# Optimization experiments

Hardware: AMD Instinct MI355X
Metric: run time of the kernel (lower is better)

The kernel has to match this reference:

```python
import jax, jax.numpy as jnp
import numpy as np

B, D_IN = 4096, 4096
TOTAL_NODES, OUT_NODES = 17384, 1000
HID = TOTAL_NODES - OUT_NODES  # 16384


def setup_inputs() -> dict:
    key = jax.random.key(0)
    k1, k2, k3, k4, k5 = jax.random.split(key, 5)
    s1 = 1.0 / np.sqrt(D_IN)
    s2 = 1.0 / np.sqrt(D_IN + HID)
    return {
        "x": jax.random.normal(k1, (B, D_IN), dtype=jnp.float32),
        "W1": jax.random.normal(k2, (HID, D_IN), dtype=jnp.float32) * s1,
        "b1": jax.random.normal(k3, (HID,), dtype=jnp.float32) * s1,
        "W2": jax.random.normal(k4, (OUT_NODES, D_IN + HID), dtype=jnp.float32) * s2,
        "b2": jax.random.normal(k5, (OUT_NODES,), dtype=jnp.float32) * s2,
    }


def reference(x, W1, b1, W2, b2):
    # layer1 + ReLU: [B, HID]
    h1 = jax.nn.relu(jnp.einsum("bd,hd->bh", x, W1) + b1)
    # concat input with hidden activations: [B, D_IN + HID]
    concat = jnp.concatenate([x, h1], axis=1)
    # layer2: [B, OUT_NODES]
    out = jnp.einsum("bc,oc->bo", concat, W2) + b2
    return out
```

## Files before the change

### kernel.cpp

```cpp
#include <hip/hip_runtime.h>
#include <cstdint>
#include <cstddef>


using u16 = unsigned short;

typedef __bf16 bf16x8 __attribute__((ext_vector_type(8)));
typedef float  f32x4  __attribute__((ext_vector_type(4)));

#define GLOBAL_AS __attribute__((address_space(1)))
#define LDS_AS    __attribute__((address_space(3)))

__device__ __forceinline__ void async_load16(const void* gp, void* lp) {
    __builtin_amdgcn_global_load_lds((GLOBAL_AS void*)gp, (LDS_AS void*)lp, 16, 0, 0);
}

__device__ __forceinline__ u16 f2bf(float f) {
    union { float f; uint32_t u; } c; c.f = f;
    uint32_t u = c.u;
    u += 0x7FFFu + ((u >> 16) & 1u);
    return (u16)(u >> 16);
}

__device__ __forceinline__ int swz(int q, int row) { return q ^ ((row >> 1) & 3); }


__global__ void cvt_x_kernel(const float* __restrict__ x, u16* __restrict__ dst) {
    int idx = blockIdx.x * 256 + threadIdx.x;
    int row = idx >> 10;
    int c4  = (idx & 1023) << 2;
    float4 v = *(const float4*)&x[(size_t)row * 4096 + c4];
    ushort4 o;
    o.x = f2bf(v.x); o.y = f2bf(v.y); o.z = f2bf(v.z); o.w = f2bf(v.w);
    *(ushort4*)&dst[(size_t)row * 20480 + c4] = o;
}

__global__ void cvt_flat_kernel(const float* __restrict__ src, u16* __restrict__ dst) {
    int idx = blockIdx.x * 256 + threadIdx.x;
    float4 v = *(const float4*)&src[(size_t)idx * 4];
    ushort4 o;
    o.x = f2bf(v.x); o.y = f2bf(v.y); o.z = f2bf(v.z); o.w = f2bf(v.w);
    *(ushort4*)&dst[(size_t)idx * 4] = o;
}

__global__ void cvt_w2_kernel(const float* __restrict__ src, u16* __restrict__ dst) {
    int idx = blockIdx.x * 256 + threadIdx.x;
    int row = idx / 5120;
    int c4  = (idx % 5120) * 4;
    ushort4 o;
    if (row < 1000) {
        float4 v = *(const float4*)&src[(size_t)row * 20480 + c4];
        o.x = f2bf(v.x); o.y = f2bf(v.y); o.z = f2bf(v.z); o.w = f2bf(v.w);
    } else {
        o.x = 0; o.y = 0; o.z = 0; o.w = 0;
    }
    *(ushort4*)&dst[(size_t)row * 20480 + c4] = o;
}

template <int EPI, int SWZ>
__global__ __launch_bounds__(512, 2)
void gemm256_kernel(const u16* __restrict__ A, int lda,
                    const u16* __restrict__ B, int ldb,
                    int K,
                    const float* __restrict__ bias,
                    void* __restrict__ Cout, int ldc, size_t c_slab) {
    __shared__ __align__(16) u16 As[4 * 8192];
    __shared__ __align__(16) u16 Bs[4 * 8192];

    const int tid = threadIdx.x;

    int bx = blockIdx.x, by = blockIdx.y;
    if (SWZ) {
        const int lin   = by * (int)gridDim.x + bx;
        const int xcd   = lin & 7;
        const int wg    = xcd * 128 + (lin >> 3);
        const int panel = wg >> 6;
        const int within = wg & 63;
        bx = (panel >> 1) * 8 + (within & 7);
        by = (panel & 1) * 8 + (within >> 3);
    }
    const int m0 = by * 256;
    const int n0 = bx * 256;
    const int kz = blockIdx.z;

    A += (size_t)kz * K;
    B += (size_t)kz * K;

    const int sr = tid >> 2;
    const int sq = tid & 3;
    const int qg = swz(sq, sr);
    const u16* ga0 = A + (size_t)(m0 + sr) * lda + qg * 8;
    const u16* ga1 = ga0 + (size_t)128 * lda;
    const u16* gb0 = B + (size_t)(n0 + sr) * ldb + qg * 8;
    const u16* gb1 = gb0 + (size_t)128 * ldb;

#define STAGE4(cb) do {                                  \
        async_load16(ga0, &As[(cb) + tid * 8]);          \
        async_load16(ga1, &As[(cb) + 4096 + tid * 8]);   \
        async_load16(gb0, &Bs[(cb) + tid * 8]);          \
        async_load16(gb1, &Bs[(cb) + 4096 + tid * 8]);   \
        ga0 += 32; ga1 += 32; gb0 += 32; gb1 += 32;      \
    } while (0)

    const int wave = tid >> 6;
    const int wm   = wave >> 2;
    const int wn   = wave & 3;
    const int lane = tid & 63;
    const int ln16 = lane & 15;
    const int quad = lane >> 4;

    int aoff[8], boff[4];
#pragma unroll
    for (int i = 0; i < 8; ++i) {
        const int ra = wm * 128 + i * 16 + ln16;
        aoff[i] = ra * 32 + swz(quad, ra) * 8;
    }
#pragma unroll
    for (int j = 0; j < 4; ++j) {
        const int rb = wn * 64 + j * 16 + ln16;
        boff[j] = rb * 32 + swz(quad, rb) * 8;
    }

    f32x4 acc[8][4] = {};

    STAGE4(0);
    STAGE4(8192);
    STAGE4(16384);

    const int NT = K >> 5;
    for (int t = 0; t < NT; ++t) {
        if (t < NT - 2)       asm volatile("s_waitcnt vmcnt(8)" ::: "memory");
        else if (t == NT - 2) asm volatile("s_waitcnt vmcnt(4)" ::: "memory");
        else                  asm volatile("s_waitcnt vmcnt(0)" ::: "memory");
        asm volatile("s_barrier" ::: "memory");

        const int cb = (t & 3) * 8192;
        bf16x8 a[8], b[4];
#pragma unroll
        for (int i = 0; i < 8; ++i) a[i] = *(const bf16x8*)&As[cb + aoff[i]];
#pragma unroll
        for (int j = 0; j < 4; ++j) b[j] = *(const bf16x8*)&Bs[cb + boff[j]];

        if (t + 3 < NT) STAGE4(((t + 3) & 3) * 8192);

        __builtin_amdgcn_s_setprio(1);
#pragma unroll
        for (int i = 0; i < 8; ++i)
#pragma unroll
            for (int j = 0; j < 4; ++j)
                acc[i][j] = __builtin_amdgcn_mfma_f32_16x16x32_bf16(
                    a[i], b[j], acc[i][j], 0, 0, 0);
        __builtin_amdgcn_s_setprio(0);

        asm volatile("s_barrier" ::: "memory");
    }
#undef STAGE4

    if (EPI == 0) {
        u16* C = (u16*)Cout;
#pragma unroll
        for (int j = 0; j < 4; ++j) {
            const int col = n0 + wn * 64 + j * 16 + ln16;
            const float bv = bias[col];
#pragma unroll
            for (int i = 0; i < 8; ++i) {
#pragma unroll
                for (int r = 0; r < 4; ++r) {
                    const int row = m0 + wm * 128 + i * 16 + quad * 4 + r;
                    float v = acc[i][j][r] + bv;
                    v = v > 0.0f ? v : 0.0f;
                    C[(size_t)row * ldc + col] = f2bf(v);
                }
            }
        }
    } else {
        float* C = (float*)Cout + (size_t)kz * c_slab;
#pragma unroll
        for (int j = 0; j < 4; ++j) {
            const int col = n0 + wn * 64 + j * 16 + ln16;
#pragma unroll
            for (int i = 0; i < 8; ++i) {
#pragma unroll
                for (int r = 0; r < 4; ++r) {
                    const int row = m0 + wm * 128 + i * 16 + quad * 4 + r;
                    C[(size_t)row * ldc + col] = acc[i][j][r];
                }
            }
        }
    }
}

__global__ void reduce_out_kernel(const float* __restrict__ part,
                                  const float* __restrict__ b2,
                                  float* __restrict__ out) {
    const int idx = blockIdx.x * 256 + threadIdx.x;
    const int m  = idx / 250;
    const int n4 = (idx % 250) * 4;
    const size_t slab = (size_t)4096 * 1024;
    const size_t off = (size_t)m * 1024 + n4;
    float4 s  = *(const float4*)&part[off];
    float4 p1 = *(const float4*)&part[slab + off];
    float4 p2 = *(const float4*)&part[2 * slab + off];
    float4 p3 = *(const float4*)&part[3 * slab + off];
    float4 bv = *(const float4*)&b2[n4];
    s.x += p1.x + p2.x + p3.x + bv.x;
    s.y += p1.y + p2.y + p3.y + bv.y;
    s.z += p1.z + p2.z + p3.z + bv.z;
    s.w += p1.w + p2.w + p3.w + bv.w;
    *(float4*)&out[(size_t)m * 1000 + n4] = s;
}


extern "C" void kernel_launch(void* const* d_in, const int* in_sizes, int n_in,
                              void* d_out, int out_size, void* d_ws, size_t ws_size,
                              hipStream_t stream) {
    const float* x  = (const float*)d_in[0];
    const float* W1 = (const float*)d_in[1];
    const float* b1 = (const float*)d_in[2];
    const float* W2 = (const float*)d_in[3];
    const float* b2 = (const float*)d_in[4];
    float* out = (float*)d_out;

    u16* concat = (u16*)d_ws;
    u16* W1b = concat + (size_t)4096 * 20480;
    u16* W2b = W1b + (size_t)16384 * 4096;
    float* partials = (float*)W1b;

    cvt_x_kernel   <<<16384, 256, 0, stream>>>(x, concat);
    cvt_flat_kernel<<<65536, 256, 0, stream>>>(W1, W1b);
    cvt_w2_kernel  <<<20480, 256, 0, stream>>>(W2, W2b);

    dim3 g1(16384 / 256, 4096 / 256, 1);
    gemm256_kernel<0, 1><<<g1, 512, 0, stream>>>(
        concat, 20480, W1b, 4096, 4096, b1, concat + 4096, 20480, 0);

    dim3 g2(1024 / 256, 4096 / 256, 4);
    gemm256_kernel<1, 0><<<g2, 512, 0, stream>>>(
        concat, 20480, W2b, 20480, 5120, nullptr, partials, 1024,
        (size_t)4096 * 1024);

    reduce_out_kernel<<<4000, 256, 0, stream>>>(partials, b2, out);
}
```

Baseline: 1.169 ms.

## Restructure GEMM main loop into K=64 ping-pong stages with interleaved quadrant MFMAs

The GEMM kernel now stages 64-wide K tiles in two LDS buffers instead of four 32-wide ones. Each iteration is split into four MFMA quadrants, with LDS fragment reads and async global loads interleaved between barriers so that memory traffic overlaps compute. The LDS swizzle changes to an 8-way XOR pattern for the wider rows, and GEMM2 gets an XCD-aware block remap. The extra barriers per iteration add synchronisation cost, and the deeper fragment buffering raises register pressure.

```diff
diff --git a/kernel.cpp b/kernel.cpp
--- a/kernel.cpp
+++ b/kernel.cpp
@@ -21,8 +21,6 @@
     u += 0x7FFFu + ((u >> 16) & 1u);
     return (u16)(u >> 16);
 }
-
-__device__ __forceinline__ int swz(int q, int row) { return q ^ ((row >> 1) & 3); }
 
 
 __global__ void cvt_x_kernel(const float* __restrict__ x, u16* __restrict__ dst) {
@@ -57,27 +55,55 @@
     *(ushort4*)&dst[(size_t)row * 20480 + c4] = o;
 }
 
+#define BAR()  asm volatile("s_barrier" ::: "memory")
+
+#define STG(P, L64, DST) do {                        \
+        async_load16(P,       (DST) + dof);          \
+        async_load16(P + L64, (DST) + 4096 + dof);   \
+        P += 64; } while (0)
+
+#define MFMA_Q(IB, JB, BF) do {                                               \
+        __builtin_amdgcn_s_setprio(1);                                       \
+        _Pragma("unroll")                                                    \
+        for (int i = 0; i < 4; ++i)                                          \
+            _Pragma("unroll")                                                \
+            for (int j = 0; j < 2; ++j) {                                    \
+                acc[(IB) + i][(JB) + j] =                                    \
+                    __builtin_amdgcn_mfma_f32_16x16x32_bf16(                 \
+                        aF[i][0], BF[j][0], acc[(IB) + i][(JB) + j], 0, 0, 0);\
+                acc[(IB) + i][(JB) + j] =                                    \
+                    __builtin_amdgcn_mfma_f32_16x16x32_bf16(                 \
+                        aF[i][1], BF[j][1], acc[(IB) + i][(JB) + j], 0, 0, 0);\
+            }                                                                \
+        __builtin_amdgcn_s_setprio(0); } while (0)
+
 template <int EPI, int SWZ>
-__global__ __launch_bounds__(512, 2)
-void gemm256_kernel(const u16* __restrict__ A, int lda,
-                    const u16* __restrict__ B, int ldb,
-                    int K,
-                    const float* __restrict__ bias,
-                    void* __restrict__ Cout, int ldc, size_t c_slab) {
-    __shared__ __align__(16) u16 As[4 * 8192];
-    __shared__ __align__(16) u16 Bs[4 * 8192];
+__device__ __forceinline__
+void gemm256p_body(const u16* __restrict__ A, int lda,
+                   const u16* __restrict__ B, int ldb,
+                   int K,
+                   const float* __restrict__ bias,
+                   void* __restrict__ Cout, int ldc, size_t c_slab) {
+    __shared__ __align__(16) u16 As[32768];
+    __shared__ __align__(16) u16 Bs[32768];
 
     const int tid = threadIdx.x;
 
     int bx = blockIdx.x, by = blockIdx.y;
-    if (SWZ) {
-        const int lin   = by * (int)gridDim.x + bx;
-        const int xcd   = lin & 7;
-        const int wg    = xcd * 128 + (lin >> 3);
-        const int panel = wg >> 6;
+    if (SWZ == 1) {
+        const int lin    = by * (int)gridDim.x + bx;
+        const int xcd    = lin & 7;
+        const int wg     = xcd * 128 + (lin >> 3);
+        const int panel  = wg >> 6;
         const int within = wg & 63;
         bx = (panel >> 1) * 8 + (within & 7);
         by = (panel & 1) * 8 + (within >> 3);
+    } else if (SWZ == 2) {
+        const int lin = by * (int)gridDim.x + bx;
+        const int xcd = lin & 7;
+        const int wg  = xcd * 8 + (lin >> 3);
+        bx = wg & 3;
+        by = wg >> 2;
     }
     const int m0 = by * 256;
     const int n0 = bx * 256;
@@ -86,21 +112,15 @@
     A += (size_t)kz * K;
     B += (size_t)kz * K;
 
-    const int sr = tid >> 2;
-    const int sq = tid & 3;
-    const int qg = swz(sq, sr);
-    const u16* ga0 = A + (size_t)(m0 + sr) * lda + qg * 8;
-    const u16* ga1 = ga0 + (size_t)128 * lda;
-    const u16* gb0 = B + (size_t)(n0 + sr) * ldb + qg * 8;
-    const u16* gb1 = gb0 + (size_t)128 * ldb;
-
-#define STAGE4(cb) do {                                  \
-        async_load16(ga0, &As[(cb) + tid * 8]);          \
-        async_load16(ga1, &As[(cb) + 4096 + tid * 8]);   \
-        async_load16(gb0, &Bs[(cb) + tid * 8]);          \
-        async_load16(gb1, &Bs[(cb) + 4096 + tid * 8]);   \
-        ga0 += 32; ga1 += 32; gb0 += 32; gb1 += 32;      \
-    } while (0)
+    const int srow = tid >> 3;
+    const int gq   = (tid & 7) ^ (srow & 7);
+    const u16* pAlo = A + (size_t)(m0 + srow) * lda + gq * 8;
+    const u16* pAhi = pAlo + (size_t)128 * lda;
+    const u16* pBlo = B + (size_t)(n0 + srow) * ldb + gq * 8;
+    const u16* pBhi = pBlo + (size_t)128 * ldb;
+    const size_t a64 = (size_t)64 * lda;
+    const size_t b64 = (size_t)64 * ldb;
+    const int dof = tid * 8;
 
     const int wave = tid >> 6;
     const int wm   = wave >> 2;
@@ -109,52 +129,82 @@
     const int ln16 = lane & 15;
     const int quad = lane >> 4;
 
-    int aoff[8], boff[4];
+    const int p0 = (quad ^ (ln16 & 7)) * 8;
+    int ao[8], bo[4];
 #pragma unroll
     for (int i = 0; i < 8; ++i) {
-        const int ra = wm * 128 + i * 16 + ln16;
-        aoff[i] = ra * 32 + swz(quad, ra) * 8;
+        const int R = wm * 128 + i * 16 + ln16;
+        ao[i] = (R >> 7) * 8192 + (R & 127) * 64 + p0;
     }
 #pragma unroll
     for (int j = 0; j < 4; ++j) {
-        const int rb = wn * 64 + j * 16 + ln16;
-        boff[j] = rb * 32 + swz(quad, rb) * 8;
+        const int R = wn * 64 + j * 16 + ln16;
+        bo[j] = (R >> 7) * 8192 + (R & 127) * 64 + p0;
     }
 
     f32x4 acc[8][4] = {};
-
-    STAGE4(0);
-    STAGE4(8192);
-    STAGE4(16384);
-
-    const int NT = K >> 5;
+    bf16x8 aF[4][2], bn0[2][2], bn1[2][2];
+
+    STG(pAlo, a64, As + 0);
+    STG(pAhi, a64, As + 8192);
+    STG(pBlo, b64, Bs + 0);
+    STG(pBhi, b64, Bs + 8192);
+    STG(pBlo, b64, Bs + 16384);
+    STG(pAlo, a64, As + 16384);
+    STG(pAhi, a64, As + 16384 + 8192);
+    asm volatile("s_waitcnt vmcnt(6)" ::: "memory");
+    BAR();
+
+    const int NT = K >> 6;
     for (int t = 0; t < NT; ++t) {
-        if (t < NT - 2)       asm volatile("s_waitcnt vmcnt(8)" ::: "memory");
-        else if (t == NT - 2) asm volatile("s_waitcnt vmcnt(4)" ::: "memory");
-        else                  asm volatile("s_waitcnt vmcnt(0)" ::: "memory");
-        asm volatile("s_barrier" ::: "memory");
-
-        const int cb = (t & 3) * 8192;
-        bf16x8 a[8], b[4];
-#pragma unroll
-        for (int i = 0; i < 8; ++i) a[i] = *(const bf16x8*)&As[cb + aoff[i]];
-#pragma unroll
-        for (int j = 0; j < 4; ++j) b[j] = *(const bf16x8*)&Bs[cb + boff[j]];
-
-        if (t + 3 < NT) STAGE4(((t + 3) & 3) * 8192);
-
-        __builtin_amdgcn_s_setprio(1);
-#pragma unroll
-        for (int i = 0; i < 8; ++i)
-#pragma unroll
-            for (int j = 0; j < 4; ++j)
-                acc[i][j] = __builtin_amdgcn_mfma_f32_16x16x32_bf16(
-                    a[i], b[j], acc[i][j], 0, 0, 0);
-        __builtin_amdgcn_s_setprio(0);
-
-        asm volatile("s_barrier" ::: "memory");
-    }
-#undef STAGE4
+        const int par  = (t & 1) << 14;
+        const int parn = 16384 - par;
+
+#pragma unroll
+        for (int i = 0; i < 4; ++i) {
+            aF[i][0] = *(const bf16x8*)&As[par + ao[i]];
+            aF[i][1] = *(const bf16x8*)&As[par + (ao[i] ^ 32)];
+        }
+#pragma unroll
+        for (int j = 0; j < 2; ++j) {
+            bn0[j][0] = *(const bf16x8*)&Bs[par + bo[j]];
+            bn0[j][1] = *(const bf16x8*)&Bs[par + (bo[j] ^ 32)];
+        }
+        if (t + 1 < NT) STG(pBhi, b64, Bs + parn + 8192);
+        BAR();
+        MFMA_Q(0, 0, bn0);
+        BAR();
+
+#pragma unroll
+        for (int j = 0; j < 2; ++j) {
+            bn1[j][0] = *(const bf16x8*)&Bs[par + bo[2 + j]];
+            bn1[j][1] = *(const bf16x8*)&Bs[par + (bo[2 + j] ^ 32)];
+        }
+        BAR();
+        MFMA_Q(0, 2, bn1);
+        BAR();
+
+#pragma unroll
+        for (int i = 0; i < 4; ++i) {
+            aF[i][0] = *(const bf16x8*)&As[par + ao[4 + i]];
+            aF[i][1] = *(const bf16x8*)&As[par + (ao[4 + i] ^ 32)];
+        }
+        if (t + 2 < NT) STG(pBlo, b64, Bs + par);
+        BAR();
+        MFMA_Q(4, 2, bn1);
+        BAR();
+
+        if (t + 2 < NT) {
+            STG(pAlo, a64, As + par);
+            STG(pAhi, a64, As + par + 8192);
+        }
+        MFMA_Q(4, 0, bn0);
+        if (t < NT - 2)
+            asm volatile("s_waitcnt vmcnt(6)" ::: "memory");
+        else if (t == NT - 2)
+            asm volatile("s_waitcnt vmcnt(0)" ::: "memory");
+        BAR();
+    }
 
     if (EPI == 0) {
         u16* C = (u16*)Cout;
@@ -188,6 +238,22 @@
             }
         }
     }
+}
+
+__global__ __launch_bounds__(512, 2)
+void gemm1_kernel(const u16* __restrict__ A, int lda,
+                  const u16* __restrict__ B, int ldb, int K,
+                  const float* __restrict__ bias,
+                  void* __restrict__ Cout, int ldc, size_t c_slab) {
+    gemm256p_body<0, 1>(A, lda, B, ldb, K, bias, Cout, ldc, c_slab);
+}
+
+__global__ __launch_bounds__(512, 2)
+void gemm2_kernel(const u16* __restrict__ A, int lda,
+                  const u16* __restrict__ B, int ldb, int K,
+                  const float* __restrict__ bias,
+                  void* __restrict__ Cout, int ldc, size_t c_slab) {
+    gemm256p_body<1, 2>(A, lda, B, ldb, K, bias, Cout, ldc, c_slab);
 }
 
 __global__ void reduce_out_kernel(const float* __restrict__ part,
@@ -231,11 +297,11 @@
     cvt_w2_kernel  <<<20480, 256, 0, stream>>>(W2, W2b);
 
     dim3 g1(16384 / 256, 4096 / 256, 1);
-    gemm256_kernel<0, 1><<<g1, 512, 0, stream>>>(
+    gemm1_kernel<<<g1, 512, 0, stream>>>(
         concat, 20480, W1b, 4096, 4096, b1, concat + 4096, 20480, 0);
 
     dim3 g2(1024 / 256, 4096 / 256, 4);
-    gemm256_kernel<1, 0><<<g2, 512, 0, stream>>>(
+    gemm2_kernel<<<g2, 512, 0, stream>>>(
         concat, 20480, W2b, 20480, 5120, nullptr, partials, 1024,
         (size_t)4096 * 1024);
 
```

Result: slower. 1.211 ms (+3.6%).
